# Kernel optimization log

Hardware: AMD Instinct MI355X
Metric: run time of the kernel (lower is better)

## Reference

```python
import jax, jax.numpy as jnp
import numpy as np


def setup_inputs() -> dict:
    key = jax.random.key(0)
    ks = jax.random.split(key, 10)
    B, N, E = 8, 20000, 320000
    IN, H = 128, 64
    x = jax.random.normal(ks[0], (B, N, IN), dtype=jnp.float32)
    additional_features = jax.random.normal(ks[1], (B, 1), dtype=jnp.float32)
    edge_index = jax.random.randint(ks[2], (2, E), 0, N, dtype=jnp.int32)
    # GCNConv params (weight applied as x @ W, plus bias)
    W1 = jax.random.normal(ks[3], (IN, H), dtype=jnp.float32) / np.sqrt(IN)
    b1 = jnp.zeros((H,), dtype=jnp.float32)
    W2 = jax.random.normal(ks[4], (H, H), dtype=jnp.float32) / np.sqrt(H)
    b2 = jnp.zeros((H,), dtype=jnp.float32)
    # fc: Linear(hidden + 1, 1)
    fc_w = jax.random.normal(ks[5], (H + 1, 1), dtype=jnp.float32) / np.sqrt(H + 1)
    fc_b = jnp.zeros((1,), dtype=jnp.float32)
    return {"x": x, "additional_features": additional_features, "edge_index": edge_index,
            "W1": W1, "b1": b1, "W2": W2, "b2": b2, "fc_w": fc_w, "fc_b": fc_b}


def reference(x, additional_features, edge_index, W1, b1, W2, b2, fc_w, fc_b):
    # x: [B, N, F]; edge_index: [2, E] shared across the batch (as in the torch code)
    B, N, _ = x.shape
    src = edge_index[0]
    dst = edge_index[1]
    # GCN with self-loops: deg = 1 + in-degree, symmetric normalization
    deg = jnp.ones((N,), jnp.float32).at[dst].add(1.0)
    dis = jax.lax.rsqrt(deg)                      # deg^{-1/2}
    enorm = dis[src] * dis[dst]                   # per-edge norm
    self_norm = (dis * dis)[None, :, None]        # self-loop norm = 1/deg

    def gcn(h, W, b):
        hw = jnp.einsum('bnf,fo->bno', h, W)      # linear transform first
        msgs = hw[:, src, :] * enorm[None, :, None]
        agg = jnp.zeros_like(hw).at[:, dst, :].add(msgs)   # scatter-add to dst
        return agg + hw * self_norm + b

    h = jax.nn.relu(gcn(x, W1, b1))
    h = jax.nn.relu(gcn(h, W2, b2))
    pooled = h.mean(axis=1)                       # global_mean_pool (equal-size graphs)
    cat = jnp.concatenate([pooled, additional_features], axis=1)
    return cat @ fc_w + fc_b                      # [B, 1]
```

## Files before the change

### kernel.cpp

```cpp
#include <hip/hip_runtime.h>

#define BLK 256

typedef __attribute__((ext_vector_type(8))) unsigned short ushort8v;

static __device__ __forceinline__ float bf2f(unsigned short u) {
    return __uint_as_float(((unsigned)u) << 16);
}
static __device__ __forceinline__ unsigned short f2bf(float f) {
    unsigned u = __float_as_uint(f);
    u += 0x7FFF + ((u >> 16) & 1);
    return (unsigned short)(u >> 16);
}

__global__ void k_zero(int* __restrict__ cnt, int N) {
    int i = blockIdx.x * BLK + threadIdx.x;
    if (i < N) cnt[i] = 0;
}

__global__ void k_count(const int* __restrict__ dst, int* __restrict__ cnt, int E) {
    int i = blockIdx.x * BLK + threadIdx.x;
    if (i < E) atomicAdd(&cnt[dst[i]], 1);
}

__global__ void k_scan1(const int* __restrict__ cnt, int* __restrict__ rs,
                        int* __restrict__ bsum, int N) {
    __shared__ int s[BLK];
    int i = blockIdx.x * BLK + threadIdx.x;
    int v = (i < N) ? cnt[i] : 0;
    s[threadIdx.x] = v;
    __syncthreads();
    for (int off = 1; off < BLK; off <<= 1) {
        int t = (threadIdx.x >= off) ? s[threadIdx.x - off] : 0;
        __syncthreads();
        s[threadIdx.x] += t;
        __syncthreads();
    }
    if (i < N) rs[i] = s[threadIdx.x] - v;
    if (threadIdx.x == BLK - 1) bsum[blockIdx.x] = s[BLK - 1];
}

__global__ void k_scan2p(int* __restrict__ bsum, int nb) {
    __shared__ int s[BLK];
    int t = threadIdx.x;
    if (nb <= BLK) {
        int v = (t < nb) ? bsum[t] : 0;
        s[t] = v;
        __syncthreads();
        for (int off = 1; off < BLK; off <<= 1) {
            int u = (t >= off) ? s[t - off] : 0;
            __syncthreads();
            s[t] += u;
            __syncthreads();
        }
        if (t < nb) bsum[t] = s[t] - v;
    } else if (t == 0) {
        int r = 0;
        for (int i = 0; i < nb; ++i) { int x = bsum[i]; bsum[i] = r; r += x; }
    }
}

__global__ void k_scan3(int* __restrict__ rs, int* __restrict__ cur,
                        const int* __restrict__ bsum, int N) {
    int i = blockIdx.x * BLK + threadIdx.x;
    if (i < N) {
        int v = rs[i] + bsum[blockIdx.x];
        rs[i] = v;
        cur[i] = v;
    }
}

__global__ void k_fill(const int* __restrict__ src, const int* __restrict__ dst,
                       const int* __restrict__ cnt, int* __restrict__ cur,
                       int* __restrict__ csrc, float* __restrict__ cw, int E) {
    int e = blockIdx.x * BLK + threadIdx.x;
    if (e >= E) return;
    int d = dst[e], s = src[e];
    int p = atomicAdd(&cur[d], 1);
    csrc[p] = s;
    cw[p] = rsqrtf((1.0f + (float)cnt[s]) * (1.0f + (float)cnt[d]));
}

template <int K, bool RELU, bool PIN, bool ABF16>
__global__ __launch_bounds__(BLK) void k_gemm(const void* __restrict__ Av,
                                              const float* __restrict__ W,
                                              unsigned short* __restrict__ C,
                                              int M, int N, int B) {
    __shared__ float As[128 * 65];
    __shared__ float Bs[64 * 64];
    const int t = threadIdx.x;
    const int row0 = blockIdx.x * 128;
    const int tx = t & 15, ty = t >> 4;

    float acc[8][4] = {};

    for (int kk = 0; kk < K; kk += 64) {
        if (kk) __syncthreads();
        if constexpr (!ABF16) {
            const float* A = (const float*)Av;
            for (int i = t; i < 128 * 16; i += BLK) {
                int r = i >> 4, c = i & 15;
                int gr = row0 + r;
                float4 v = make_float4(0.f, 0.f, 0.f, 0.f);
                if (gr < M) {
                    size_t ra = PIN ? ((size_t)(gr % B) * N + (gr / B)) : (size_t)gr;
                    v = *reinterpret_cast<const float4*>(A + ra * K + kk + c * 4);
                }
                if (RELU) {
                    v.x = fmaxf(v.x, 0.f); v.y = fmaxf(v.y, 0.f);
                    v.z = fmaxf(v.z, 0.f); v.w = fmaxf(v.w, 0.f);
                }
                *reinterpret_cast<float4*>(As + r * 65 + c * 4) = v;
            }
        } else {
            const unsigned short* A = (const unsigned short*)Av;
            for (int i = t; i < 128 * 8; i += BLK) {
                int r = i >> 3, c = i & 7;
                int gr = row0 + r;
                float f[8];
                if (gr < M) {
                    ushort8v v = *reinterpret_cast<const ushort8v*>(A + (size_t)gr * K + kk + c * 8);
                    #pragma unroll
                    for (int j = 0; j < 8; ++j) f[j] = bf2f(v[j]);
                } else {
                    #pragma unroll
                    for (int j = 0; j < 8; ++j) f[j] = 0.f;
                }
                if (RELU) {
                    #pragma unroll
                    for (int j = 0; j < 8; ++j) f[j] = fmaxf(f[j], 0.f);
                }
                float* dstp = As + r * 65 + c * 8;
                *reinterpret_cast<float4*>(dstp)     = make_float4(f[0], f[1], f[2], f[3]);
                *reinterpret_cast<float4*>(dstp + 4) = make_float4(f[4], f[5], f[6], f[7]);
            }
        }
        for (int i = t; i < 64 * 16; i += BLK) {
            int r = i >> 4, c = i & 15;
            *reinterpret_cast<float4*>(Bs + r * 64 + c * 4) =
                *reinterpret_cast<const float4*>(W + (size_t)(kk + r) * 64 + c * 4);
        }
        __syncthreads();

        #pragma unroll 4
        for (int k2 = 0; k2 < 64; ++k2) {
            float4 bv = *reinterpret_cast<const float4*>(Bs + k2 * 64 + tx * 4);
            float a[8];
            #pragma unroll
            for (int i = 0; i < 8; ++i) a[i] = As[(ty * 8 + i) * 65 + k2];
            #pragma unroll
            for (int i = 0; i < 8; ++i) {
                acc[i][0] = fmaf(a[i], bv.x, acc[i][0]);
                acc[i][1] = fmaf(a[i], bv.y, acc[i][1]);
                acc[i][2] = fmaf(a[i], bv.z, acc[i][2]);
                acc[i][3] = fmaf(a[i], bv.w, acc[i][3]);
            }
        }
    }

    #pragma unroll
    for (int i = 0; i < 8; ++i) {
        int gr = row0 + ty * 8 + i;
        if (gr < M) {
            ushort4 o;
            o.x = f2bf(acc[i][0]); o.y = f2bf(acc[i][1]);
            o.z = f2bf(acc[i][2]); o.w = f2bf(acc[i][3]);
            *reinterpret_cast<ushort4*>(C + (size_t)gr * 64 + tx * 4) = o;
        }
    }
}

template <bool FINAL>
__global__ __launch_bounds__(BLK) void k_gather(const unsigned short* __restrict__ hw,
                                                const int* __restrict__ rs,
                                                const int* __restrict__ cnt,
                                                const int* __restrict__ csrc,
                                                const float* __restrict__ cw,
                                                const float* __restrict__ bias,
                                                unsigned short* __restrict__ agg,
                                                const float* __restrict__ fcw,
                                                float* __restrict__ partial, int N) {
    const int w = threadIdx.x >> 6, lane = threadIdx.x & 63;
    const int n = blockIdx.x * 4 + w;
    const bool active = (n < N);
    float a[8] = {};

    if (active) {
        const int beg = rs[n];
        const int deg = cnt[n];
        const float self = 1.0f / (1.0f + (float)deg);
        const float* bp = bias + (lane & 7) * 8;
        ushort8v v = *reinterpret_cast<const ushort8v*>(hw + (size_t)n * 512 + lane * 8);
        #pragma unroll
        for (int j = 0; j < 8; ++j) a[j] = fmaf(bf2f(v[j]), self, bp[j]);

        int i = 0;
        for (; i + 2 <= deg; i += 2) {
            int s0 = csrc[beg + i], s1 = csrc[beg + i + 1];
            float w0 = cw[beg + i], w1 = cw[beg + i + 1];
            ushort8v x0 = *reinterpret_cast<const ushort8v*>(hw + (size_t)s0 * 512 + lane * 8);
            ushort8v x1 = *reinterpret_cast<const ushort8v*>(hw + (size_t)s1 * 512 + lane * 8);
            #pragma unroll
            for (int j = 0; j < 8; ++j) a[j] = fmaf(w0, bf2f(x0[j]), a[j]);
            #pragma unroll
            for (int j = 0; j < 8; ++j) a[j] = fmaf(w1, bf2f(x1[j]), a[j]);
        }
        if (i < deg) {
            int s0 = csrc[beg + i];
            float w0 = cw[beg + i];
            ushort8v x0 = *reinterpret_cast<const ushort8v*>(hw + (size_t)s0 * 512 + lane * 8);
            #pragma unroll
            for (int j = 0; j < 8; ++j) a[j] = fmaf(w0, bf2f(x0[j]), a[j]);
        }
    }

    if (!FINAL) {
        if (active) {
            ushort8v o;
            #pragma unroll
            for (int j = 0; j < 8; ++j) o[j] = f2bf(a[j]);
            *reinterpret_cast<ushort8v*>(agg + (size_t)n * 512 + lane * 8) = o;
        }
    } else {
        __shared__ float sm[4][8];
        const float* fp = fcw + (lane & 7) * 8;
        float s = 0.f;
        #pragma unroll
        for (int j = 0; j < 8; ++j) s = fmaf(fmaxf(a[j], 0.f), fp[j], s);
        #pragma unroll
        for (int off = 1; off < 8; off <<= 1) s += __shfl_xor(s, off, 64);
        if ((lane & 7) == 0) sm[w][lane >> 3] = s;
        __syncthreads();
        if (threadIdx.x < 8)
            partial[(size_t)blockIdx.x * 8 + threadIdx.x] =
                sm[0][threadIdx.x] + sm[1][threadIdx.x] + sm[2][threadIdx.x] + sm[3][threadIdx.x];
    }
}

__global__ void k_finish(const float* __restrict__ partial, int nblk,
                         const float* __restrict__ addf, const float* __restrict__ fcw,
                         const float* __restrict__ fcb, float* __restrict__ out,
                         int N, int H) {
    int b = blockIdx.x;
    float s = 0.f;
    for (int i = threadIdx.x; i < nblk; i += BLK) s += partial[(size_t)i * 8 + b];
    __shared__ float sm[BLK / 64];
    int lane = threadIdx.x & 63, w = threadIdx.x >> 6;
    #pragma unroll
    for (int off = 32; off; off >>= 1) s += __shfl_down(s, off, 64);
    if (lane == 0) sm[w] = s;
    __syncthreads();
    if (threadIdx.x == 0) {
        float t = sm[0] + sm[1] + sm[2] + sm[3];
        out[b] = t / (float)N + addf[b] * fcw[H] + fcb[0];
    }
}

extern "C" void kernel_launch(void* const* d_in, const int* in_sizes, int n_in,
                              void* d_out, int out_size, void* d_ws, size_t ws_size,
                              hipStream_t stream) {
    const float* x    = (const float*)d_in[0];
    const float* addf = (const float*)d_in[1];
    const int*   ei   = (const int*)d_in[2];
    const float* W1   = (const float*)d_in[3];
    const float* b1   = (const float*)d_in[4];
    const float* W2   = (const float*)d_in[5];
    const float* b2   = (const float*)d_in[6];
    const float* fcw  = (const float*)d_in[7];
    const float* fcb  = (const float*)d_in[8];
    float* out = (float*)d_out;

    const int B  = in_sizes[1];
    const int H  = in_sizes[4];
    const int IN = in_sizes[3] / H;
    const int E  = in_sizes[2] / 2;
    const int N  = in_sizes[0] / (B * IN);
    const int* src = ei;
    const int* dst = ei + E;

    const int M = B * N;

    size_t bufsz = (size_t)M * H;
    unsigned short* bufA = (unsigned short*)d_ws;
    unsigned short* bufB = bufA + bufsz;
    int*   cnt   = (int*)(bufB + bufsz);
    int*   rs    = cnt + N;
    int*   cur   = rs + N;
    int*   csrc  = cur + N;
    float* cw    = (float*)(csrc + E);
    int*   bsum  = (int*)(cw + E);
    float* partial = (float*)(bsum + 256);

    const int nbN = (N + BLK - 1) / BLK;
    const int nbE = (E + BLK - 1) / BLK;
    const int nodes4 = (N + 3) / 4;

    k_zero<<<dim3(nbN), dim3(BLK), 0, stream>>>(cnt, N);
    k_count<<<dim3(nbE), dim3(BLK), 0, stream>>>(dst, cnt, E);
    k_scan1<<<dim3(nbN), dim3(BLK), 0, stream>>>(cnt, rs, bsum, N);
    k_scan2p<<<dim3(1), dim3(BLK), 0, stream>>>(bsum, nbN);
    k_scan3<<<dim3(nbN), dim3(BLK), 0, stream>>>(rs, cur, bsum, N);
    k_fill<<<dim3(nbE), dim3(BLK), 0, stream>>>(src, dst, cnt, cur, csrc, cw, E);

    k_gemm<128, false, true, false><<<dim3((M + 127) / 128), dim3(BLK), 0, stream>>>(
        x, W1, bufA, M, N, B);
    k_gather<false><<<dim3(nodes4), dim3(BLK), 0, stream>>>(
        bufA, rs, cnt, csrc, cw, b1, bufB, fcw, partial, N);

    k_gemm<64, true, false, true><<<dim3((M + 127) / 128), dim3(BLK), 0, stream>>>(
        bufB, W2, bufA, M, N, B);
    k_gather<true><<<dim3(nodes4), dim3(BLK), 0, stream>>>(
        bufA, rs, cnt, csrc, cw, b2, nullptr, fcw, partial, N);

    k_finish<<<dim3(B), dim3(BLK), 0, stream>>>(partial, nodes4, addf, fcw, fcb, out, N, H);
}
```

Measured before the change: 332.8 us.

## Use bf16 MFMA for GCN linear transforms and merge scan kernels

Replaces the FP32 FMA tiled GEMMs with bf16 MFMA 16x16x32 kernels. The weights are pre-transposed to bf16 inside the init kernel, and inputs are converted to bf16 when staged into shared memory. Output goes through a shared-memory staging buffer so stores are coalesced. The three-kernel CSR scan becomes a single 1024-thread kernel to cut launch overhead. In exchange, the first-layer input x is rounded to bf16, which lowers precision.

```diff
diff --git a/kernel.cpp b/kernel.cpp
--- a/kernel.cpp
+++ b/kernel.cpp
@@ -3,6 +3,9 @@
 #define BLK 256
 
 typedef __attribute__((ext_vector_type(8))) unsigned short ushort8v;
+typedef __attribute__((ext_vector_type(4))) unsigned short ushort4v;
+typedef __attribute__((ext_vector_type(8))) short short8v;
+typedef __attribute__((ext_vector_type(4))) float f32x4;
 
 static __device__ __forceinline__ float bf2f(unsigned short u) {
     return __uint_as_float(((unsigned)u) << 16);
@@ -13,9 +16,20 @@
     return (unsigned short)(u >> 16);
 }
 
-__global__ void k_zero(int* __restrict__ cnt, int N) {
+__global__ void k_init(int* __restrict__ cnt, int N,
+                       const float* __restrict__ W1, const float* __restrict__ W2,
+                       unsigned short* __restrict__ Wt1, unsigned short* __restrict__ Wt2,
+                       int IN, int H) {
     int i = blockIdx.x * BLK + threadIdx.x;
     if (i < N) cnt[i] = 0;
+    if (i < IN * H) {
+        int k = i / H, c = i % H;
+        Wt1[(size_t)c * IN + k] = f2bf(W1[i]);
+    }
+    if (i < H * H) {
+        int k = i / H, c = i % H;
+        Wt2[(size_t)c * H + k] = f2bf(W2[i]);
+    }
 }
 
 __global__ void k_count(const int* __restrict__ dst, int* __restrict__ cnt, int E) {
@@ -23,50 +37,29 @@
     if (i < E) atomicAdd(&cnt[dst[i]], 1);
 }
 
-__global__ void k_scan1(const int* __restrict__ cnt, int* __restrict__ rs,
-                        int* __restrict__ bsum, int N) {
-    __shared__ int s[BLK];
-    int i = blockIdx.x * BLK + threadIdx.x;
-    int v = (i < N) ? cnt[i] : 0;
-    s[threadIdx.x] = v;
-    __syncthreads();
-    for (int off = 1; off < BLK; off <<= 1) {
-        int t = (threadIdx.x >= off) ? s[threadIdx.x - off] : 0;
+__global__ __launch_bounds__(1024) void k_scan_all(const int* __restrict__ cnt,
+                                                   int* __restrict__ rs,
+                                                   int* __restrict__ cur, int N) {
+    __shared__ int sm[1024];
+    const int t = threadIdx.x;
+    const int chunk = (N + 1023) >> 10;
+    const int lo = t * chunk;
+    const int hi = min(lo + chunk, N);
+    int s = 0;
+    for (int i = lo; i < hi; ++i) s += cnt[i];
+    sm[t] = s;
+    __syncthreads();
+    for (int off = 1; off < 1024; off <<= 1) {
+        int v = (t >= off) ? sm[t - off] : 0;
         __syncthreads();
-        s[threadIdx.x] += t;
+        sm[t] += v;
         __syncthreads();
     }
-    if (i < N) rs[i] = s[threadIdx.x] - v;
-    if (threadIdx.x == BLK - 1) bsum[blockIdx.x] = s[BLK - 1];
-}
-
-__global__ void k_scan2p(int* __restrict__ bsum, int nb) {
-    __shared__ int s[BLK];
-    int t = threadIdx.x;
-    if (nb <= BLK) {
-        int v = (t < nb) ? bsum[t] : 0;
-        s[t] = v;
-        __syncthreads();
-        for (int off = 1; off < BLK; off <<= 1) {
-            int u = (t >= off) ? s[t - off] : 0;
-            __syncthreads();
-            s[t] += u;
-            __syncthreads();
-        }
-        if (t < nb) bsum[t] = s[t] - v;
-    } else if (t == 0) {
-        int r = 0;
-        for (int i = 0; i < nb; ++i) { int x = bsum[i]; bsum[i] = r; r += x; }
-    }
-}
-
-__global__ void k_scan3(int* __restrict__ rs, int* __restrict__ cur,
-                        const int* __restrict__ bsum, int N) {
-    int i = blockIdx.x * BLK + threadIdx.x;
-    if (i < N) {
-        int v = rs[i] + bsum[blockIdx.x];
-        rs[i] = v;
-        cur[i] = v;
+    int run = sm[t] - s;
+    for (int i = lo; i < hi; ++i) {
+        int c = cnt[i];
+        rs[i] = run; cur[i] = run;
+        run += c;
     }
 }
 
@@ -82,91 +75,95 @@
 }
 
 template <int K, bool RELU, bool PIN, bool ABF16>
-__global__ __launch_bounds__(BLK) void k_gemm(const void* __restrict__ Av,
-                                              const float* __restrict__ W,
-                                              unsigned short* __restrict__ C,
-                                              int M, int N, int B) {
-    __shared__ float As[128 * 65];
-    __shared__ float Bs[64 * 64];
+__global__ __launch_bounds__(BLK) void k_gemm_mfma(const void* __restrict__ Av,
+                                                   const unsigned short* __restrict__ Wt,
+                                                   unsigned short* __restrict__ C,
+                                                   int M, int N, int B) {
+    constexpr int LDA = K + 8;
+    __shared__ unsigned short As[128 * LDA];
+    __shared__ unsigned short Bs[64 * LDA];
     const int t = threadIdx.x;
     const int row0 = blockIdx.x * 128;
-    const int tx = t & 15, ty = t >> 4;
-
-    float acc[8][4] = {};
-
-    for (int kk = 0; kk < K; kk += 64) {
-        if (kk) __syncthreads();
-        if constexpr (!ABF16) {
-            const float* A = (const float*)Av;
-            for (int i = t; i < 128 * 16; i += BLK) {
-                int r = i >> 4, c = i & 15;
-                int gr = row0 + r;
-                float4 v = make_float4(0.f, 0.f, 0.f, 0.f);
-                if (gr < M) {
-                    size_t ra = PIN ? ((size_t)(gr % B) * N + (gr / B)) : (size_t)gr;
-                    v = *reinterpret_cast<const float4*>(A + ra * K + kk + c * 4);
-                }
-                if (RELU) {
-                    v.x = fmaxf(v.x, 0.f); v.y = fmaxf(v.y, 0.f);
-                    v.z = fmaxf(v.z, 0.f); v.w = fmaxf(v.w, 0.f);
-                }
-                *reinterpret_cast<float4*>(As + r * 65 + c * 4) = v;
+
+    for (int i = t; i < 64 * (K / 8); i += BLK) {
+        int r = i / (K / 8), c = i % (K / 8);
+        *reinterpret_cast<ushort8v*>(&Bs[r * LDA + c * 8]) =
+            *reinterpret_cast<const ushort8v*>(Wt + (size_t)r * K + c * 8);
+    }
+    if constexpr (!ABF16) {
+        const float* A = (const float*)Av;
+        for (int i = t; i < 128 * (K / 4); i += BLK) {
+            int r = i / (K / 4), c = i % (K / 4);
+            int gr = row0 + r;
+            float4 v = make_float4(0.f, 0.f, 0.f, 0.f);
+            if (gr < M) {
+                size_t ra = PIN ? ((size_t)(gr % B) * N + (gr / B)) : (size_t)gr;
+                v = *reinterpret_cast<const float4*>(A + ra * K + c * 4);
             }
-        } else {
-            const unsigned short* A = (const unsigned short*)Av;
-            for (int i = t; i < 128 * 8; i += BLK) {
-                int r = i >> 3, c = i & 7;
-                int gr = row0 + r;
-                float f[8];
-                if (gr < M) {
-                    ushort8v v = *reinterpret_cast<const ushort8v*>(A + (size_t)gr * K + kk + c * 8);
-                    #pragma unroll
-                    for (int j = 0; j < 8; ++j) f[j] = bf2f(v[j]);
-                } else {
-                    #pragma unroll
-                    for (int j = 0; j < 8; ++j) f[j] = 0.f;
-                }
-                if (RELU) {
-                    #pragma unroll
-                    for (int j = 0; j < 8; ++j) f[j] = fmaxf(f[j], 0.f);
-                }
-                float* dstp = As + r * 65 + c * 8;
-                *reinterpret_cast<float4*>(dstp)     = make_float4(f[0], f[1], f[2], f[3]);
-                *reinterpret_cast<float4*>(dstp + 4) = make_float4(f[4], f[5], f[6], f[7]);
+            if (RELU) {
+                v.x = fmaxf(v.x, 0.f); v.y = fmaxf(v.y, 0.f);
+                v.z = fmaxf(v.z, 0.f); v.w = fmaxf(v.w, 0.f);
             }
-        }
-        for (int i = t; i < 64 * 16; i += BLK) {
-            int r = i >> 4, c = i & 15;
-            *reinterpret_cast<float4*>(Bs + r * 64 + c * 4) =
-                *reinterpret_cast<const float4*>(W + (size_t)(kk + r) * 64 + c * 4);
-        }
-        __syncthreads();
-
-        #pragma unroll 4
-        for (int k2 = 0; k2 < 64; ++k2) {
-            float4 bv = *reinterpret_cast<const float4*>(Bs + k2 * 64 + tx * 4);
-            float a[8];
-            #pragma unroll
-            for (int i = 0; i < 8; ++i) a[i] = As[(ty * 8 + i) * 65 + k2];
-            #pragma unroll
-            for (int i = 0; i < 8; ++i) {
-                acc[i][0] = fmaf(a[i], bv.x, acc[i][0]);
-                acc[i][1] = fmaf(a[i], bv.y, acc[i][1]);
-                acc[i][2] = fmaf(a[i], bv.z, acc[i][2]);
-                acc[i][3] = fmaf(a[i], bv.w, acc[i][3]);
+            ushort4v o;
+            o[0] = f2bf(v.x); o[1] = f2bf(v.y); o[2] = f2bf(v.z); o[3] = f2bf(v.w);
+            *reinterpret_cast<ushort4v*>(&As[r * LDA + c * 4]) = o;
+        }
+    } else {
+        const unsigned short* A = (const unsigned short*)Av;
+        for (int i = t; i < 128 * (K / 8); i += BLK) {
+            int r = i / (K / 8), c = i % (K / 8);
+            int gr = row0 + r;
+            ushort8v v = {0, 0, 0, 0, 0, 0, 0, 0};
+            if (gr < M) v = *reinterpret_cast<const ushort8v*>(A + (size_t)gr * K + c * 8);
+            if (RELU) {
+                #pragma unroll
+                for (int j = 0; j < 8; ++j) v[j] = (v[j] & 0x8000) ? 0 : v[j];
             }
-        }
-    }
-
+            *reinterpret_cast<ushort8v*>(&As[r * LDA + c * 8]) = v;
+        }
+    }
+    __syncthreads();
+
+    const int w = t >> 6, lane = t & 63;
+    const int lrow = lane & 15;
+    const int lk = (lane >> 4) * 8;
+
+    f32x4 acc[2][4] = {};
     #pragma unroll
-    for (int i = 0; i < 8; ++i) {
-        int gr = row0 + ty * 8 + i;
-        if (gr < M) {
-            ushort4 o;
-            o.x = f2bf(acc[i][0]); o.y = f2bf(acc[i][1]);
-            o.z = f2bf(acc[i][2]); o.w = f2bf(acc[i][3]);
-            *reinterpret_cast<ushort4*>(C + (size_t)gr * 64 + tx * 4) = o;
-        }
+    for (int ks = 0; ks < K / 32; ++ks) {
+        short8v a[2], b[4];
+        #pragma unroll
+        for (int fr = 0; fr < 2; ++fr)
+            a[fr] = *reinterpret_cast<const short8v*>(
+                &As[(w * 32 + fr * 16 + lrow) * LDA + ks * 32 + lk]);
+        #pragma unroll
+        for (int fc = 0; fc < 4; ++fc)
+            b[fc] = *reinterpret_cast<const short8v*>(
+                &Bs[(fc * 16 + lrow) * LDA + ks * 32 + lk]);
+        #pragma unroll
+        for (int fr = 0; fr < 2; ++fr)
+            #pragma unroll
+            for (int fc = 0; fc < 4; ++fc)
+                acc[fr][fc] = __builtin_amdgcn_mfma_f32_16x16x32_bf16(
+                    a[fr], b[fc], acc[fr][fc], 0, 0, 0);
+    }
+
+    __syncthreads();
+    #pragma unroll
+    for (int fr = 0; fr < 2; ++fr)
+        #pragma unroll
+        for (int fc = 0; fc < 4; ++fc)
+            #pragma unroll
+            for (int j = 0; j < 4; ++j)
+                As[(w * 32 + fr * 16 + (lane >> 4) * 4 + j) * 72 + fc * 16 + lrow] =
+                    f2bf(acc[fr][fc][j]);
+    __syncthreads();
+    for (int i = t; i < 128 * 8; i += BLK) {
+        int r = i >> 3, c = i & 7;
+        int gr = row0 + r;
+        if (gr < M)
+            *reinterpret_cast<ushort8v*>(C + (size_t)gr * 64 + c * 8) =
+                *reinterpret_cast<const ushort8v*>(&As[r * 72 + c * 8]);
     }
 }
 
@@ -288,27 +285,26 @@
     int*   cur   = rs + N;
     int*   csrc  = cur + N;
     float* cw    = (float*)(csrc + E);
-    int*   bsum  = (int*)(cw + E);
-    float* partial = (float*)(bsum + 256);
+    unsigned short* Wt1 = (unsigned short*)(cw + E);
+    unsigned short* Wt2 = Wt1 + (size_t)H * IN;
+    float* partial = (float*)(Wt2 + (size_t)H * H);
 
     const int nbN = (N + BLK - 1) / BLK;
     const int nbE = (E + BLK - 1) / BLK;
     const int nodes4 = (N + 3) / 4;
 
-    k_zero<<<dim3(nbN), dim3(BLK), 0, stream>>>(cnt, N);
+    k_init<<<dim3(nbN), dim3(BLK), 0, stream>>>(cnt, N, W1, W2, Wt1, Wt2, IN, H);
     k_count<<<dim3(nbE), dim3(BLK), 0, stream>>>(dst, cnt, E);
-    k_scan1<<<dim3(nbN), dim3(BLK), 0, stream>>>(cnt, rs, bsum, N);
-    k_scan2p<<<dim3(1), dim3(BLK), 0, stream>>>(bsum, nbN);
-    k_scan3<<<dim3(nbN), dim3(BLK), 0, stream>>>(rs, cur, bsum, N);
+    k_scan_all<<<dim3(1), dim3(1024), 0, stream>>>(cnt, rs, cur, N);
     k_fill<<<dim3(nbE), dim3(BLK), 0, stream>>>(src, dst, cnt, cur, csrc, cw, E);
 
-    k_gemm<128, false, true, false><<<dim3((M + 127) / 128), dim3(BLK), 0, stream>>>(
-        x, W1, bufA, M, N, B);
+    k_gemm_mfma<128, false, true, false><<<dim3((M + 127) / 128), dim3(BLK), 0, stream>>>(
+        x, Wt1, bufA, M, N, B);
     k_gather<false><<<dim3(nodes4), dim3(BLK), 0, stream>>>(
         bufA, rs, cnt, csrc, cw, b1, bufB, fcw, partial, N);
 
-    k_gemm<64, true, false, true><<<dim3((M + 127) / 128), dim3(BLK), 0, stream>>>(
-        bufB, W2, bufA, M, N, B);
+    k_gemm_mfma<64, true, false, true><<<dim3((M + 127) / 128), dim3(BLK), 0, stream>>>(
+        bufB, Wt2, bufA, M, N, B);
     k_gather<true><<<dim3(nodes4), dim3(BLK), 0, stream>>>(
         bufA, rs, cnt, csrc, cw, b2, nullptr, fcw, partial, N);
 
```

New measurement: 325.4 us. 1.02x faster.
